# Kernel tuning notes

Measured on AMD Instinct MI355X. Metric: run time of the kernel, lower is better.

The kernel has to match this reference:

```python
import jax, jax.numpy as jnp
import numpy as np

POLY_DEGREE = 2
LEVELS = 3


def setup_inputs() -> dict:
    key = jax.random.key(0)
    B, T, C = 32, 4096, 128
    x = jax.random.normal(key, (B, T, C), dtype=jnp.float32)
    return {"x": x}


def reference(x):
    B, T, C = x.shape
    t = jnp.linspace(0.0, 1.0, T, dtype=x.dtype)[:, None]          # [T,1]
    Tmat = jnp.concatenate([t ** i for i in range(POLY_DEGREE + 1)], axis=1)  # [T,d+1]
    # Least-squares solution is identical across batch & channel since the
    # design matrix is shared: sol = pinv(Tmat) @ x  (closed-form, one solve).
    P = jnp.linalg.pinv(Tmat)                                       # [d+1,T]
    coef = jnp.einsum('dt,btc->bdc', P, x)                          # [B,d+1,C]
    low = jnp.einsum('td,bdc->btc', Tmat, coef)                     # [B,T,C] trend
    res = x - low                                                   # residual
    highs = [res] + [jnp.zeros_like(res) for _ in range(LEVELS - 1)]
    return (low, highs)
```

## Files before the change

### kernel.cpp

```cpp
#include <hip/hip_runtime.h>

typedef float f4 __attribute__((ext_vector_type(4)));

#define TT 4096
#define CC 128
#define BB 32
#define C4 (CC / 4)
#define NGM 16
#define SLAB (TT / NGM)
#define NTILE 64

__global__ __launch_bounds__(256) void k_moments(const f4* __restrict__ x4,
                                                 f4* __restrict__ partial,
                                                 float scale) {
    const int blk = blockIdx.x;
    const int tid = threadIdx.x;
    const int r = tid >> 5;
    const int q = tid & 31;
    const int b = blk >> 4;
    const int s = blk & 15;
    const f4* xb = x4 + (size_t)b * TT * C4;
    const int t0 = s * SLAB;

    f4 m0 = (f4)0.0f, m1 = (f4)0.0f, m2 = (f4)0.0f;
#pragma unroll 8
    for (int k = 0; k < SLAB / 8; ++k) {
        const int t = t0 + r + (k << 3);
        const float u = fmaf((float)t, scale, -0.5f);
        const f4 v = xb[(size_t)t * C4 + q];
        m0 += v;
        m1 += u * v;
        m2 += (u * u) * v;
    }

    __shared__ f4 red[3][8][32];
    red[0][r][q] = m0;
    red[1][r][q] = m1;
    red[2][r][q] = m2;
    __syncthreads();

    if (tid < 32) {
#pragma unroll
        for (int j = 0; j < 3; ++j) {
            f4 acc = red[j][0][tid];
#pragma unroll
            for (int rr = 1; rr < 8; ++rr) acc += red[j][rr][tid];
            partial[(size_t)blk * (3 * C4) + j * C4 + tid] = acc;
        }
    }
}

template <bool FUSE_ZERO>
__global__ __launch_bounds__(256) void k_emit_all(const f4* __restrict__ x4,
                                                  const f4* __restrict__ partial,
                                                  f4* __restrict__ out,
                                                  float scale, float c20,
                                                  float invS0, float invS2,
                                                  float invD) {
    const size_t N4 = (size_t)BB * TT * C4;
    const int blk = blockIdx.x;
    const int b = blk >> 6;
    const int tile = blk & 63;
    const int tid = threadIdx.x;
    const int r = tid >> 5;
    const int q = tid & 31;

    __shared__ f4 red[3][8][32];
    __shared__ f4 ca[3][32];

    const f4* pb = partial + (size_t)b * (NGM * 3 * C4);
#pragma unroll
    for (int j = 0; j < 3; ++j) {
        const f4 e0 = pb[(size_t)(2 * r + 0) * (3 * C4) + j * C4 + q];
        const f4 e1 = pb[(size_t)(2 * r + 1) * (3 * C4) + j * C4 + q];
        red[j][r][q] = e0 + e1;
    }
    __syncthreads();
    if (tid < 32) {
        f4 s0 = (f4)0.0f, s1 = (f4)0.0f, s2 = (f4)0.0f;
#pragma unroll
        for (int rr = 0; rr < 8; ++rr) {
            s0 += red[0][rr][tid];
            s1 += red[1][rr][tid];
            s2 += red[2][rr][tid];
        }
        ca[0][tid] = s0 * invS0;
        ca[1][tid] = s1 * invS2;
        ca[2][tid] = (s2 - c20 * s0) * invD;
    }
    __syncthreads();

    const f4 a0 = ca[0][q];
    const f4 a1 = ca[1][q];
    const f4 a2 = ca[2][q];
    const f4 z = (f4)0.0f;

    const size_t base = (size_t)b * TT * C4;
    const int t0 = tile * 64;
#pragma unroll
    for (int k = 0; k < 8; ++k) {
        const int t = t0 + r + (k << 3);
        const float u = fmaf((float)t, scale, -0.5f);
        const float w = fmaf(u, u, -c20);
        const size_t idx = base + (size_t)t * C4 + q;
        const f4 xv = x4[idx];
        const f4 lo = a0 + u * a1 + w * a2;
        const f4 re = xv - lo;
        __builtin_nontemporal_store(lo, &out[idx]);
        __builtin_nontemporal_store(re, &out[N4 + idx]);
        if (FUSE_ZERO) {
            __builtin_nontemporal_store(z, &out[2 * N4 + idx]);
            __builtin_nontemporal_store(z, &out[3 * N4 + idx]);
        }
    }
}

extern "C" void kernel_launch(void* const* d_in, const int* in_sizes, int n_in,
                              void* d_out, int out_size, void* d_ws, size_t ws_size,
                              hipStream_t stream) {
    const float* x = (const float*)d_in[0];
    float* out = (float*)d_out;
    const size_t N = (size_t)BB * TT * CC;

    double S0 = (double)TT, S2 = 0.0, S4 = 0.0;
    for (int i = 0; i < TT; ++i) {
        double u = (double)i / (double)(TT - 1) - 0.5;
        double u2 = u * u;
        S2 += u2;
        S4 += u2 * u2;
    }
    const double c20d = S2 / S0;
    const double Dd = S4 - S2 * S2 / S0;
    const float scale = (float)(1.0 / (double)(TT - 1));
    const float invS0 = (float)(1.0 / S0);
    const float invS2 = (float)(1.0 / S2);
    const float invD  = (float)(1.0 / Dd);
    const float c20   = (float)c20d;

    const size_t partial_elems = (size_t)BB * NGM * 3 * C4;
    const size_t need_bytes    = partial_elems * sizeof(f4);

    if (ws_size >= need_bytes) {
        f4* partial = (f4*)d_ws;
        k_moments<<<BB * NGM, 256, 0, stream>>>((const f4*)x, partial, scale);
        k_emit_all<true><<<BB * NTILE, 256, 0, stream>>>(
            (const f4*)x, partial, (f4*)out, scale, c20, invS0, invS2, invD);
    } else {
        f4* partial = (f4*)(out + 2 * N);
        k_moments<<<BB * NGM, 256, 0, stream>>>((const f4*)x, partial, scale);
        k_emit_all<false><<<BB * NTILE, 256, 0, stream>>>(
            (const f4*)x, partial, (f4*)out, scale, c20, invS0, invS2, invD);
        hipMemsetAsync(out + 2 * N, 0, 2 * N * sizeof(float), stream);
    }
}
```

Before: 65.21 us.

## Move zero-fill of extra outputs into moments kernel and drop nontemporal stores

Zero-filling the two all-zero output levels moves from the emit kernel into extra blocks of the moments kernel. The memory-bound moments reduction, which uses few blocks, can then overlap with the zero writes, and the emit kernel only writes low and residual. The nontemporal stores in the emit kernel also become ordinary stores. This changes cache behaviour for the stores, and the shared-memory declaration now sits inside a branch, so the __syncthreads is reached only by moments blocks.

```diff
diff --git a/kernel.cpp b/kernel.cpp
--- a/kernel.cpp
+++ b/kernel.cpp
@@ -10,53 +10,66 @@
 #define SLAB (TT / NGM)
 #define NTILE 64
 
-__global__ __launch_bounds__(256) void k_moments(const f4* __restrict__ x4,
-                                                 f4* __restrict__ partial,
-                                                 float scale) {
+__global__ __launch_bounds__(256) void k_moments_zero(const f4* __restrict__ x4,
+                                                      f4* __restrict__ partial,
+                                                      f4* __restrict__ out,
+                                                      float scale) {
+    const size_t N4 = (size_t)BB * TT * C4;
     const int blk = blockIdx.x;
     const int tid = threadIdx.x;
     const int r = tid >> 5;
     const int q = tid & 31;
-    const int b = blk >> 4;
-    const int s = blk & 15;
-    const f4* xb = x4 + (size_t)b * TT * C4;
-    const int t0 = s * SLAB;
 
-    f4 m0 = (f4)0.0f, m1 = (f4)0.0f, m2 = (f4)0.0f;
+    if (blk < BB * NGM) {
+        const int b = blk >> 4;
+        const int s = blk & 15;
+        const f4* xb = x4 + (size_t)b * TT * C4;
+        const int t0 = s * SLAB;
+        f4 m0 = (f4)0.0f, m1 = (f4)0.0f, m2 = (f4)0.0f;
 #pragma unroll 8
-    for (int k = 0; k < SLAB / 8; ++k) {
-        const int t = t0 + r + (k << 3);
-        const float u = fmaf((float)t, scale, -0.5f);
-        const f4 v = xb[(size_t)t * C4 + q];
-        m0 += v;
-        m1 += u * v;
-        m2 += (u * u) * v;
-    }
-
-    __shared__ f4 red[3][8][32];
-    red[0][r][q] = m0;
-    red[1][r][q] = m1;
-    red[2][r][q] = m2;
-    __syncthreads();
-
-    if (tid < 32) {
+        for (int k = 0; k < SLAB / 8; ++k) {
+            const int t = t0 + r + (k << 3);
+            const float u = fmaf((float)t, scale, -0.5f);
+            const f4 v = xb[(size_t)t * C4 + q];
+            m0 += v;
+            m1 += u * v;
+            m2 += (u * u) * v;
+        }
+        __shared__ f4 red[3][8][32];
+        red[0][r][q] = m0;
+        red[1][r][q] = m1;
+        red[2][r][q] = m2;
+        __syncthreads();
+        if (tid < 32) {
 #pragma unroll
-        for (int j = 0; j < 3; ++j) {
-            f4 acc = red[j][0][tid];
+            for (int j = 0; j < 3; ++j) {
+                f4 acc = red[j][0][tid];
 #pragma unroll
-            for (int rr = 1; rr < 8; ++rr) acc += red[j][rr][tid];
-            partial[(size_t)blk * (3 * C4) + j * C4 + tid] = acc;
+                for (int rr = 1; rr < 8; ++rr) acc += red[j][rr][tid];
+                partial[(size_t)blk * (3 * C4) + j * C4 + tid] = acc;
+            }
+        }
+    } else {
+        const int zid = blk - BB * NGM;
+        const int b = zid >> 6;
+        const int tile = zid & 63;
+        const size_t base = (size_t)b * TT * C4 + (size_t)(tile * 64) * C4;
+        const f4 z = (f4)0.0f;
+#pragma unroll
+        for (int k = 0; k < 8; ++k) {
+            const size_t idx = base + (size_t)(r + (k << 3)) * C4 + q;
+            out[2 * N4 + idx] = z;
+            out[3 * N4 + idx] = z;
         }
     }
 }
 
-template <bool FUSE_ZERO>
-__global__ __launch_bounds__(256) void k_emit_all(const f4* __restrict__ x4,
-                                                  const f4* __restrict__ partial,
-                                                  f4* __restrict__ out,
-                                                  float scale, float c20,
-                                                  float invS0, float invS2,
-                                                  float invD) {
+__global__ __launch_bounds__(256) void k_emit(const f4* __restrict__ x4,
+                                              const f4* __restrict__ partial,
+                                              f4* __restrict__ out,
+                                              float scale, float c20,
+                                              float invS0, float invS2,
+                                              float invD) {
     const size_t N4 = (size_t)BB * TT * C4;
     const int blk = blockIdx.x;
     const int b = blk >> 6;
@@ -93,7 +106,6 @@
     const f4 a0 = ca[0][q];
     const f4 a1 = ca[1][q];
     const f4 a2 = ca[2][q];
-    const f4 z = (f4)0.0f;
 
     const size_t base = (size_t)b * TT * C4;
     const int t0 = tile * 64;
@@ -106,12 +118,8 @@
         const f4 xv = x4[idx];
         const f4 lo = a0 + u * a1 + w * a2;
         const f4 re = xv - lo;
-        __builtin_nontemporal_store(lo, &out[idx]);
-        __builtin_nontemporal_store(re, &out[N4 + idx]);
-        if (FUSE_ZERO) {
-            __builtin_nontemporal_store(z, &out[2 * N4 + idx]);
-            __builtin_nontemporal_store(z, &out[3 * N4 + idx]);
-        }
+        out[idx] = lo;
+        out[N4 + idx] = re;
     }
 }
 
@@ -142,13 +150,15 @@
 
     if (ws_size >= need_bytes) {
         f4* partial = (f4*)d_ws;
-        k_moments<<<BB * NGM, 256, 0, stream>>>((const f4*)x, partial, scale);
-        k_emit_all<true><<<BB * NTILE, 256, 0, stream>>>(
+        k_moments_zero<<<BB * NGM + BB * NTILE, 256, 0, stream>>>(
+            (const f4*)x, partial, (f4*)out, scale);
+        k_emit<<<BB * NTILE, 256, 0, stream>>>(
             (const f4*)x, partial, (f4*)out, scale, c20, invS0, invS2, invD);
     } else {
         f4* partial = (f4*)(out + 2 * N);
-        k_moments<<<BB * NGM, 256, 0, stream>>>((const f4*)x, partial, scale);
-        k_emit_all<false><<<BB * NTILE, 256, 0, stream>>>(
+        k_moments_zero<<<BB * NGM, 256, 0, stream>>>(
+            (const f4*)x, partial, (f4*)out, scale);
+        k_emit<<<BB * NTILE, 256, 0, stream>>>(
             (const f4*)x, partial, (f4*)out, scale, c20, invS0, invS2, invD);
         hipMemsetAsync(out + 2 * N, 0, 2 * N * sizeof(float), stream);
     }
```

Result: faster. 62.98 us (-3.4%).
